# Performance work log

Measured on AMD Instinct MI355X. Metric: run time of the kernel, lower is better.

## Reference

```python
import jax, jax.numpy as jnp
import numpy as np

D, W, B, T = 128, 512, 512, 512

# Tsit5 Butcher tableau (Tsitouras 2011), as used by diffrax.Tsit5
A21 = 0.161
A31, A32 = -0.008480655492356989, 0.335480655492357
A41, A42, A43 = 2.8971530571054935, -6.359448489975075, 4.3622954328695815
A51, A52, A53, A54 = 5.325864828439257, -11.748883564062828, 7.4955393428898365, -0.09249506636175525
A61, A62, A63, A64, A65 = 5.86145544294642, -12.92096931784711, 8.159367898576159, -0.071584973281401, -0.028269050394068383
B1, B2, B3, B4, B5, B6 = 0.09646076681806523, 0.01, 0.4798896504144996, 1.379008574103742, -3.290069515436081, 2.324710524099774


def setup_inputs() -> dict:
    key = jax.random.key(0)
    ks = jax.random.split(key, 8)
    u = lambda k, shape, s: jax.random.uniform(k, shape, minval=-s, maxval=s, dtype=jnp.float32)
    s3 = float(np.sqrt(1.0 / 3.0))
    sD = float(1.0 / np.sqrt(D))
    sW = float(1.0 / np.sqrt(W))
    return {
        "ts": jnp.arange(T, dtype=jnp.float32) * 1e-3,  # uniform save grid, dt0 = 1e-3
        "yi": jax.random.normal(ks[0], (B, 1, D), dtype=jnp.float32),
        "w1": u(ks[1], (W, D), sD), "b1": u(ks[2], (W,), sD),
        "w2": u(ks[3], (W, W), sW), "b2": u(ks[4], (W,), sW),
        "w3": u(ks[5], (D, W), sW), "b3": u(ks[6], (D,), sW),
        "A": u(ks[7], (D, D), s3),
    }


def reference(ts, yi, w1, b1, w2, b2, w3, b3, A):
    # StabilizedFunc: f(y) = MLP(y) + A @ y, batched over B
    def vf(y):  # y: [B, D]
        h = jnp.tanh(y @ w1.T + b1)
        h = jnp.tanh(h @ w2.T + b2)
        return h @ w3.T + b3 + y @ A.T

    def step(y, h):  # one constant-step Tsit5 step of size h
        k1 = vf(y)
        k2 = vf(y + h * (A21 * k1))
        k3 = vf(y + h * (A31 * k1 + A32 * k2))
        k4 = vf(y + h * (A41 * k1 + A42 * k2 + A43 * k3))
        k5 = vf(y + h * (A51 * k1 + A52 * k2 + A53 * k3 + A54 * k4))
        k6 = vf(y + h * (A61 * k1 + A62 * k2 + A63 * k3 + A64 * k4 + A65 * k5))
        y_new = y + h * (B1 * k1 + B2 * k2 + B3 * k3 + B4 * k4 + B5 * k5 + B6 * k6)
        return y_new, y_new

    y0 = yi[:, 0, :]                      # [B, D]
    dts = ts[1:] - ts[:-1]                # [T-1]
    _, ys = jax.lax.scan(step, y0, dts)   # ys: [T-1, B, D]
    out = jnp.concatenate([y0[None], ys], axis=0)  # [T, B, D]
    return jnp.transpose(out, (1, 0, 2))  # [B, T, D]
```

## Files before the change

kernel.cpp:

```cpp
#include <hip/hip_runtime.h>
#include <stdint.h>


#define Dd 128
#define Ww 512
#define Tt 512
#define NSTEP 511
#define NWG 32
#define NTHR 512

#define WSTR_W 40960
#define WSTAT_BASE 327680
#define WSTAT_W 10240
#define WS_TOT 409600

#define RING_W_B 12288
#define H1F 98304
#define H2F 114688
#define Y0F 131072
#define Y1F 135168
#define ATF 139264
#define DTF 139520
#define SMEMB 141568

typedef __attribute__((ext_vector_type(8))) __bf16 bf16x8;
typedef __attribute__((ext_vector_type(4))) float f32x4;

__device__ __forceinline__ unsigned short f2b(float f) {
  union { float f; unsigned int u; } v; v.f = f;
  return (unsigned short)((v.u + 0x7fffu + ((v.u >> 16) & 1u)) >> 16);
}
__device__ __forceinline__ float fast_tanh(float x) {
  x = fminf(fmaxf(x, -15.f), 15.f);
  float e = __expf(2.f * x);
  return (e - 1.f) / (e + 1.f);
}
__device__ __forceinline__ int fragaddr(int m, int n) {
  return ((n >> 5) << 10) + ((((n >> 3) & 3) * 16 + m) << 4) + ((n & 7) << 1);
}

__device__ const float RKC[48] = {
  0.161f, 0.f, 0.f, 0.f, 0.f, 0.f, 0.f, 0.f,
  -0.008480655492356989f, 0.335480655492357f, 0.f, 0.f, 0.f, 0.f, 0.f, 0.f,
  2.8971530571054935f, -6.359448489975075f, 4.3622954328695815f, 0.f, 0.f, 0.f, 0.f, 0.f,
  5.325864828439257f, -11.748883564062828f, 7.4955393428898365f,
  -0.09249506636175525f, 0.f, 0.f, 0.f, 0.f,
  5.86145544294642f, -12.92096931784711f, 8.159367898576159f,
  -0.071584973281401f, -0.028269050394068383f, 0.f, 0.f, 0.f,
  0.09646076681806523f, 0.01f, 0.4798896504144996f, 1.379008574103742f,
  -3.290069515436081f, 2.324710524099774f, 0.f, 0.f
};

#define GLDS(gp, lp) __builtin_amdgcn_global_load_lds( \
    (const __attribute__((address_space(1))) unsigned int*)(const void*)(gp), \
    (__attribute__((address_space(3))) unsigned int*)(void*)(lp), 16, 0, 0)

#define VMW8() do { asm volatile("s_waitcnt vmcnt(8)" ::: "memory"); \
                    __builtin_amdgcn_sched_barrier(0); } while (0)
#define LGKM0() do { asm volatile("s_waitcnt lgkmcnt(0)" ::: "memory"); \
                     __builtin_amdgcn_sched_barrier(0); } while (0)
#define LBAR() do { asm volatile("s_waitcnt lgkmcnt(0)" ::: "memory"); \
                    __builtin_amdgcn_s_barrier(); } while (0)

#define ISSUE4(ro_, igo_) do { \
    GLDS(gsb + (igo_),        ring_w + (ro_)); \
    GLDS(gsb + (igo_) + 1024, ring_w + (ro_) + 1024); \
    GLDS(gsb + (igo_) + 2048, ring_w + (ro_) + 2048); \
    GLDS(gsb + (igo_) + 3072, ring_w + (ro_) + 3072); } while (0)
#define ADV() do { ro  = (ro  == 8192)  ? 0 : ro  + 4096; \
                   igo = (igo == 77824) ? 0 : igo + 4096; } while (0)

#define MFMA(a, b, c) __builtin_amdgcn_mfma_f32_16x16x32_bf16((a), (b), (c), 0, 0, 0)
#define CPK(kd) do { kd[0]=kk[0]; kd[1]=kk[1]; kd[2]=kk[2]; kd[3]=kk[3]; } while (0)

__global__ void prep_kernel(const float* __restrict__ w1,
                            const float* __restrict__ w2,
                            const float* __restrict__ w3,
                            const float* __restrict__ Am,
                            unsigned short* __restrict__ wsb) {
  for (int i = blockIdx.x * blockDim.x + threadIdx.x; i < WS_TOT;
       i += gridDim.x * blockDim.x) {
    float v;
    if (i < WSTAT_BASE) {
      const int w = i / WSTR_W, r = i % WSTR_W;
      const int g = r >> 10, tile = (r >> 9) & 1;
      const int L = (r >> 3) & 63, j = r & 7;
      const int l16 = L & 15, q = L >> 4;
      if (g < 32) {
        const int nt = (g & 1) * 2 + tile, ks = g >> 1;
        v = w2[(w * 64 + nt * 16 + l16) * Ww + ks * 32 + q * 8 + j];
      } else {
        const int kcol = 2 * (g - 32) + tile;
        v = w3[(w * 16 + l16) * Ww + kcol * 32 + q * 8 + j];
      }
    } else {
      const int ii = i - WSTAT_BASE;
      const int w = ii / WSTAT_W, r = ii % WSTAT_W;
      const int idx = r >> 10, tile = (r >> 9) & 1;
      const int L = (r >> 3) & 63, j = r & 7;
      const int l16 = L & 15, q = L >> 4;
      if (idx < 8) {
        const int ks = idx >> 1, nt = (idx & 1) * 2 + tile;
        v = w1[(w * 64 + nt * 16 + l16) * Dd + ks * 32 + q * 8 + j];
      } else {
        const int kcol = 2 * (idx - 8) + tile;
        v = Am[(w * 16 + l16) * Dd + kcol * 32 + q * 8 + j];
      }
    }
    wsb[i] = f2b(v);
  }
}

__global__ void __launch_bounds__(NTHR, 1)
ode_kernel(const float* __restrict__ ts,
           const float* __restrict__ yi,
           const float* __restrict__ b1,
           const float* __restrict__ b2,
           const float* __restrict__ b3,
           float* __restrict__ out,
           const unsigned short* __restrict__ wsb)
{
  extern __shared__ char smem_c[];

  const int tid  = threadIdx.x;
  const int wid  = tid >> 6;
  const int lane = tid & 63;
  const int l16  = lane & 15;
  const int quad = lane >> 4;
  const int lob  = lane << 4;
  const int b0   = blockIdx.x * 16;

  char* ring_w = smem_c + wid * RING_W_B;
  char* h1f = smem_c + H1F;
  char* h2f = smem_c + H2F;

  const char* gsb = (const char*)(wsb + wid * WSTR_W) + (lane << 4);
  const unsigned short* wstat = wsb + WSTAT_BASE + wid * WSTAT_W;

  bf16x8 w1f[4][4];
  #pragma unroll
  for (int ks = 0; ks < 4; ++ks)
    #pragma unroll
    for (int nt = 0; nt < 4; ++nt)
      w1f[ks][nt] = *(const bf16x8*)(wstat + (2*ks + (nt>>1)) * 1024 +
                                     (nt & 1) * 512 + (lane << 3));
  bf16x8 Af[4];
  #pragma unroll
  for (int kc = 0; kc < 4; ++kc)
    Af[kc] = *(const bf16x8*)(wstat + 8192 + (kc>>1) * 1024 +
                              (kc & 1) * 512 + (lane << 3));

  if (tid < 48) *(float*)(smem_c + ATF + (tid << 2)) = RKC[tid];
  for (int i = tid; i < NSTEP; i += NTHR)
    *(float*)(smem_c + DTF + (i << 2)) = ts[i + 1] - ts[i];

  float b1v[4], b2v[4];
  #pragma unroll
  for (int nt = 0; nt < 4; ++nt) {
    b1v[nt] = b1[(wid << 6) + (nt << 4) + l16];
    b2v[nt] = b2[(wid << 6) + (nt << 4) + l16];
  }
  const float b3v = b3[(wid << 4) + l16];

  int hwaddr[4];
  #pragma unroll
  for (int nt = 0; nt < 4; ++nt)
    hwaddr[nt] = fragaddr(quad << 2, (wid << 6) + (nt << 4) + l16);
  const int nC = (wid << 4) + l16;
  const int ydst = fragaddr(quad << 2, nC);

  float y[4];
  #pragma unroll
  for (int r = 0; r < 4; ++r) {
    y[r] = yi[(size_t)(b0 + (quad << 2) + r) * Dd + nC];
    *(unsigned short*)(smem_c + Y0F + ydst + (r << 4)) = f2b(y[r]);
    out[(size_t)(b0 + (quad << 2) + r) * (Tt * Dd) + nC] = y[r];
  }

  float k0[4] = {0,0,0,0}, k1[4] = {0,0,0,0}, k2[4] = {0,0,0,0},
        k3[4] = {0,0,0,0}, k4[4] = {0,0,0,0}, k5[4] = {0,0,0,0};

  __syncthreads();

  int ro = 0, igo = 12288;
  ISSUE4(0, 0); ISSUE4(4096, 4096); ISSUE4(8192, 8192);

  #pragma unroll 1
  for (int t = 0; t < NSTEP; ++t) {
    const float hdt = *(const float*)(smem_c + DTF + (t << 2));

    #pragma unroll 1
    for (int s = 0; s < 6; ++s) {
      const char* ybr = smem_c + ((s & 1) ? Y1F : Y0F);
      char*       ybw = smem_c + ((s & 1) ? Y0F : Y1F);

      LBAR();

      {
        f32x4 accA[4];
        #pragma unroll
        for (int nt = 0; nt < 4; ++nt) { f32x4 z = {0.f,0.f,0.f,0.f}; accA[nt] = z; }
        #pragma unroll
        for (int ks = 0; ks < 4; ++ks) {
          bf16x8 af = *(const bf16x8*)(ybr + (ks << 10) + lob);
          #pragma unroll
          for (int nt = 0; nt < 4; ++nt)
            accA[nt] = MFMA(af, w1f[ks][nt], accA[nt]);
        }
        #pragma unroll
        for (int nt = 0; nt < 4; ++nt)
          #pragma unroll
          for (int r = 0; r < 4; ++r)
            *(unsigned short*)(h1f + hwaddr[nt] + (r << 4)) =
                f2b(fast_tanh(accA[nt][r] + b1v[nt]));
      }
      LBAR();

      {
        f32x4 accB[4];
        #pragma unroll
        for (int nt = 0; nt < 4; ++nt) { f32x4 z = {0.f,0.f,0.f,0.f}; accB[nt] = z; }
        #pragma unroll
        for (int ks = 0; ks < 16; ++ks) {
          VMW8();
          bf16x8 af = *(const bf16x8*)(h1f + (ks << 10) + lob);
          bf16x8 bv[4];
          #pragma unroll
          for (int nt = 0; nt < 4; ++nt)
            bv[nt] = *(const bf16x8*)(ring_w + ro + (nt << 10) + lob);
          LGKM0();
          ISSUE4(ro, igo);
          ADV();
          #pragma unroll
          for (int nt = 0; nt < 4; ++nt)
            accB[nt] = MFMA(af, bv[nt], accB[nt]);
        }
        #pragma unroll
        for (int nt = 0; nt < 4; ++nt)
          #pragma unroll
          for (int r = 0; r < 4; ++r)
            *(unsigned short*)(h2f + hwaddr[nt] + (r << 4)) =
                f2b(fast_tanh(accB[nt][r] + b2v[nt]));
      }
      LBAR();

      {
        f32x4 accC0 = {0.f, 0.f, 0.f, 0.f};
        f32x4 accC1 = {0.f, 0.f, 0.f, 0.f};
        #pragma unroll
        for (int cc = 0; cc < 4; ++cc) {
          VMW8();
          bf16x8 afv[4], bv[4];
          #pragma unroll
          for (int t4 = 0; t4 < 4; ++t4) {
            afv[t4] = *(const bf16x8*)(h2f + ((4*cc + t4) << 10) + lob);
            bv[t4]  = *(const bf16x8*)(ring_w + ro + (t4 << 10) + lob);
          }
          LGKM0();
          ISSUE4(ro, igo);
          ADV();
          accC0 = MFMA(afv[0], bv[0], accC0);
          accC1 = MFMA(afv[1], bv[1], accC1);
          accC0 = MFMA(afv[2], bv[2], accC0);
          accC1 = MFMA(afv[3], bv[3], accC1);
        }
        #pragma unroll
        for (int kc = 0; kc < 4; ++kc) {
          bf16x8 afy = *(const bf16x8*)(ybr + (kc << 10) + lob);
          if (kc & 1) accC1 = MFMA(afy, Af[kc], accC1);
          else        accC0 = MFMA(afy, Af[kc], accC0);
        }
        float kk[4];
        #pragma unroll
        for (int r = 0; r < 4; ++r) kk[r] = accC0[r] + accC1[r] + b3v;
        switch (s) {
          case 0: CPK(k0); break;
          case 1: CPK(k1); break;
          case 2: CPK(k2); break;
          case 3: CPK(k3); break;
          case 4: CPK(k4); break;
          default: CPK(k5); break;
        }
      }

      {
        const float* cp = (const float*)(smem_c + ATF + (s << 5));
        const float c0 = cp[0], c1 = cp[1], c2 = cp[2];
        const float c3 = cp[3], c4 = cp[4], c5 = cp[5];
        float a_[4];
        #pragma unroll
        for (int r = 0; r < 4; ++r)
          a_[r] = y[r] + hdt * (c0*k0[r] + c1*k1[r] + c2*k2[r] +
                                c3*k3[r] + c4*k4[r] + c5*k5[r]);
        #pragma unroll
        for (int r = 0; r < 4; ++r)
          *(unsigned short*)(ybw + ydst + (r << 4)) = f2b(a_[r]);
        if (s == 5) {
          #pragma unroll
          for (int r = 0; r < 4; ++r) {
            y[r] = a_[r];
            out[(size_t)(b0 + (quad << 2) + r) * (Tt * Dd) +
                (size_t)(t + 1) * Dd + nC] = a_[r];
          }
        }
      }
    }
  }
}

extern "C" void kernel_launch(void* const* d_in, const int* in_sizes, int n_in,
                              void* d_out, int out_size, void* d_ws, size_t ws_size,
                              hipStream_t stream) {
  (void)in_sizes; (void)n_in; (void)out_size; (void)ws_size;

  const float* ts = (const float*)d_in[0];
  const float* yi = (const float*)d_in[1];
  const float* w1 = (const float*)d_in[2];
  const float* b1 = (const float*)d_in[3];
  const float* w2 = (const float*)d_in[4];
  const float* b2 = (const float*)d_in[5];
  const float* w3 = (const float*)d_in[6];
  const float* b3 = (const float*)d_in[7];
  const float* Am = (const float*)d_in[8];
  float* outp = (float*)d_out;
  unsigned short* wsb = (unsigned short*)d_ws;

  (void)hipFuncSetAttribute(reinterpret_cast<const void*>(ode_kernel),
                            hipFuncAttributeMaxDynamicSharedMemorySize,
                            SMEMB);

  prep_kernel<<<400, 256, 0, stream>>>(w1, w2, w3, Am, wsb);
  ode_kernel<<<dim3(NWG), dim3(NTHR), SMEMB, stream>>>(
      ts, yi, b1, b2, b3, outp, wsb);
}
```

Before: 37.11 ms.

## Stream streaming weights directly into registers instead of LDS ring via global_load_lds

Replaces the per-wave LDS ring buffer filled with global_load_lds with a 4-deep register ring (bb[4][4]) loaded by ordinary global vector loads, prefetching three groups ahead. This removes the LDS round-trip and explicit vmcnt/lgkmcnt waits for weight tiles and shrinks LDS use substantially. The cost is many more VGPRs held live (64 registers of prefetched weights plus the pinned static fragments), which risks spilling or lower occupancy, and it relies on the compiler to place the vmem waits.

```diff
diff --git a/kernel.cpp b/kernel.cpp
--- a/kernel.cpp
+++ b/kernel.cpp
@@ -14,14 +14,13 @@
 #define WSTAT_W 10240
 #define WS_TOT 409600
 
-#define RING_W_B 12288
-#define H1F 98304
-#define H2F 114688
-#define Y0F 131072
-#define Y1F 135168
-#define ATF 139264
-#define DTF 139520
-#define SMEMB 141568
+#define H1F 0
+#define H2F 16384
+#define Y0F 32768
+#define Y1F 36864
+#define ATF 40960
+#define DTF 41152
+#define SMEMB 43200
 
 typedef __attribute__((ext_vector_type(8))) __bf16 bf16x8;
 typedef __attribute__((ext_vector_type(4))) float f32x4;
@@ -51,24 +50,16 @@
   -3.290069515436081f, 2.324710524099774f, 0.f, 0.f
 };
 
-#define GLDS(gp, lp) __builtin_amdgcn_global_load_lds( \
-    (const __attribute__((address_space(1))) unsigned int*)(const void*)(gp), \
-    (__attribute__((address_space(3))) unsigned int*)(void*)(lp), 16, 0, 0)
-
-#define VMW8() do { asm volatile("s_waitcnt vmcnt(8)" ::: "memory"); \
-                    __builtin_amdgcn_sched_barrier(0); } while (0)
-#define LGKM0() do { asm volatile("s_waitcnt lgkmcnt(0)" ::: "memory"); \
-                     __builtin_amdgcn_sched_barrier(0); } while (0)
+#define SRCB(mm) ((((mm) % 20)) * 4096)
+#define LDGRP(bi, mm) do { \
+    bb[bi][0] = *(const bf16x8*)(gsb + SRCB(mm)); \
+    bb[bi][1] = *(const bf16x8*)(gsb + SRCB(mm) + 1024); \
+    bb[bi][2] = *(const bf16x8*)(gsb + SRCB(mm) + 2048); \
+    bb[bi][3] = *(const bf16x8*)(gsb + SRCB(mm) + 3072); \
+  } while (0)
+
 #define LBAR() do { asm volatile("s_waitcnt lgkmcnt(0)" ::: "memory"); \
                     __builtin_amdgcn_s_barrier(); } while (0)
-
-#define ISSUE4(ro_, igo_) do { \
-    GLDS(gsb + (igo_),        ring_w + (ro_)); \
-    GLDS(gsb + (igo_) + 1024, ring_w + (ro_) + 1024); \
-    GLDS(gsb + (igo_) + 2048, ring_w + (ro_) + 2048); \
-    GLDS(gsb + (igo_) + 3072, ring_w + (ro_) + 3072); } while (0)
-#define ADV() do { ro  = (ro  == 8192)  ? 0 : ro  + 4096; \
-                   igo = (igo == 77824) ? 0 : igo + 4096; } while (0)
 
 #define MFMA(a, b, c) __builtin_amdgcn_mfma_f32_16x16x32_bf16((a), (b), (c), 0, 0, 0)
 #define CPK(kd) do { kd[0]=kk[0]; kd[1]=kk[1]; kd[2]=kk[2]; kd[3]=kk[3]; } while (0)
@@ -130,7 +121,6 @@
   const int lob  = lane << 4;
   const int b0   = blockIdx.x * 16;
 
-  char* ring_w = smem_c + wid * RING_W_B;
   char* h1f = smem_c + H1F;
   char* h2f = smem_c + H2F;
 
@@ -149,6 +139,14 @@
   for (int kc = 0; kc < 4; ++kc)
     Af[kc] = *(const bf16x8*)(wstat + 8192 + (kc>>1) * 1024 +
                               (kc & 1) * 512 + (lane << 3));
+  #pragma unroll
+  for (int ks = 0; ks < 4; ++ks)
+    #pragma unroll
+    for (int nt = 0; nt < 4; ++nt)
+      asm volatile("" : "+v"(w1f[ks][nt]));
+  #pragma unroll
+  for (int kc = 0; kc < 4; ++kc)
+    asm volatile("" : "+v"(Af[kc]));
 
   if (tid < 48) *(float*)(smem_c + ATF + (tid << 2)) = RKC[tid];
   for (int i = tid; i < NSTEP; i += NTHR)
@@ -182,8 +180,8 @@
 
   __syncthreads();
 
-  int ro = 0, igo = 12288;
-  ISSUE4(0, 0); ISSUE4(4096, 4096); ISSUE4(8192, 8192);
+  bf16x8 bb[4][4];
+  LDGRP(0, 0); LDGRP(1, 1); LDGRP(2, 2);
 
   #pragma unroll 1
   for (int t = 0; t < NSTEP; ++t) {
@@ -221,19 +219,13 @@
         #pragma unroll
         for (int nt = 0; nt < 4; ++nt) { f32x4 z = {0.f,0.f,0.f,0.f}; accB[nt] = z; }
         #pragma unroll
-        for (int ks = 0; ks < 16; ++ks) {
-          VMW8();
-          bf16x8 af = *(const bf16x8*)(h1f + (ks << 10) + lob);
-          bf16x8 bv[4];
+        for (int m = 0; m < 16; ++m) {
+          LDGRP((m + 3) & 3, m + 3);
+          __builtin_amdgcn_sched_barrier(0);
+          bf16x8 af = *(const bf16x8*)(h1f + (m << 10) + lob);
           #pragma unroll
           for (int nt = 0; nt < 4; ++nt)
-            bv[nt] = *(const bf16x8*)(ring_w + ro + (nt << 10) + lob);
-          LGKM0();
-          ISSUE4(ro, igo);
-          ADV();
-          #pragma unroll
-          for (int nt = 0; nt < 4; ++nt)
-            accB[nt] = MFMA(af, bv[nt], accB[nt]);
+            accB[nt] = MFMA(af, bb[m & 3][nt], accB[nt]);
         }
         #pragma unroll
         for (int nt = 0; nt < 4; ++nt)
@@ -249,20 +241,16 @@
         f32x4 accC1 = {0.f, 0.f, 0.f, 0.f};
         #pragma unroll
         for (int cc = 0; cc < 4; ++cc) {
-          VMW8();
-          bf16x8 afv[4], bv[4];
-          #pragma unroll
-          for (int t4 = 0; t4 < 4; ++t4) {
-            afv[t4] = *(const bf16x8*)(h2f + ((4*cc + t4) << 10) + lob);
-            bv[t4]  = *(const bf16x8*)(ring_w + ro + (t4 << 10) + lob);
-          }
-          LGKM0();
-          ISSUE4(ro, igo);
-          ADV();
-          accC0 = MFMA(afv[0], bv[0], accC0);
-          accC1 = MFMA(afv[1], bv[1], accC1);
-          accC0 = MFMA(afv[2], bv[2], accC0);
-          accC1 = MFMA(afv[3], bv[3], accC1);
+          LDGRP((19 + cc) & 3, 19 + cc);
+          __builtin_amdgcn_sched_barrier(0);
+          bf16x8 a0 = *(const bf16x8*)(h2f + ((4*cc + 0) << 10) + lob);
+          bf16x8 a1 = *(const bf16x8*)(h2f + ((4*cc + 1) << 10) + lob);
+          bf16x8 a2 = *(const bf16x8*)(h2f + ((4*cc + 2) << 10) + lob);
+          bf16x8 a3 = *(const bf16x8*)(h2f + ((4*cc + 3) << 10) + lob);
+          accC0 = MFMA(a0, bb[cc][0], accC0);
+          accC1 = MFMA(a1, bb[cc][1], accC1);
+          accC0 = MFMA(a2, bb[cc][2], accC0);
+          accC1 = MFMA(a3, bb[cc][3], accC1);
         }
         #pragma unroll
         for (int kc = 0; kc < 4; ++kc) {
```

Result: slower. 47.33 ms (+27.5%).
